# Kernel tuning notes

Hardware: AMD Instinct MI355X
Metric: run time of the kernel (lower is better)

## Reference

```python
import jax, jax.numpy as jnp
import numpy as np

N, E, D_IN, D, D_OUT = 100000, 3200000, 16, 128, 16
LN_EPS = 1e-5


def setup_inputs() -> dict:
    key = jax.random.key(0)
    ks = jax.random.split(key, 10)
    s = lambda fan_in: 1.0 / np.sqrt(fan_in)
    return {
        "X": jax.random.normal(ks[0], (N, D_IN), jnp.float32),
        "W_enc0": jax.random.uniform(ks[1], (D_IN, D), jnp.float32, -s(D_IN), s(D_IN)),
        "b_enc0": jnp.zeros((D,), jnp.float32),
        "W_enc1": jax.random.uniform(ks[2], (D, D), jnp.float32, -s(D), s(D)),
        "b_enc1": jnp.zeros((D,), jnp.float32),
        "W_conv": jax.random.uniform(ks[3], (D, D), jnp.float32, -s(D), s(D)),
        "b_conv": jnp.zeros((D,), jnp.float32),
        "ln_g": jnp.ones((D,), jnp.float32),
        "ln_b": jnp.zeros((D,), jnp.float32),
        "W_dec0": jax.random.uniform(ks[4], (D, D), jnp.float32, -s(D), s(D)),
        "b_dec0": jnp.zeros((D,), jnp.float32),
        "W_dec1": jax.random.uniform(ks[5], (D, D_OUT), jnp.float32, -s(D), s(D)),
        "b_dec1": jnp.zeros((D_OUT,), jnp.float32),
        "edge_index": jax.random.randint(ks[6], (2, E), 0, N, jnp.int64),
        "msg_steps": 3,
    }


def _layer_norm(x, g, b):
    mu = jnp.mean(x, axis=-1, keepdims=True)
    var = jnp.mean((x - mu) ** 2, axis=-1, keepdims=True)
    return (x - mu) * jax.lax.rsqrt(var + LN_EPS) * g + b


def reference(X, W_enc0, b_enc0, W_enc1, b_enc1, W_conv, b_conv, ln_g, ln_b,
              W_dec0, b_dec0, W_dec1, b_dec1, edge_index, msg_steps):
    n = X.shape[0]
    # --- PyG GCNConv normalization: add self-loops, symmetric deg norm ---
    loops = jnp.arange(n, dtype=edge_index.dtype)
    row = jnp.concatenate([edge_index[0], loops])  # source nodes [E+N]
    col = jnp.concatenate([edge_index[1], loops])  # target nodes [E+N]
    deg = jax.ops.segment_sum(jnp.ones_like(col, jnp.float32), col, num_segments=n)
    dinv = jnp.where(deg > 0, jax.lax.rsqrt(deg), 0.0)
    norm = dinv[row] * dinv[col]  # [E+N]

    # --- encoder MLP (relu between layers, none after last) ---
    x = jax.nn.relu(X @ W_enc0 + b_enc0)
    x = x @ W_enc1 + b_enc1

    # --- message-passing loop: x = LN(x + GCNConv(x)) ---
    for _ in range(msg_steps):
        h = x @ W_conv                          # [N, D] linear first (GCNConv)
        msg = h[row] * norm[:, None]            # gather + scale  [E+N, D]
        agg = jax.ops.segment_sum(msg, col, num_segments=n) + b_conv
        x = _layer_norm(x + agg, ln_g, ln_b)

    # --- decoder MLP ---
    x = jax.nn.relu(x @ W_dec0 + b_dec0)
    x = x @ W_dec1 + b_dec1
    return x
```

## Files before the change

kernel.cpp:

```cpp
#include <hip/hip_runtime.h>

#define N_NODES 100000
#define NEDGE   3200000
#define DIN     16
#define DIM     128
#define DOUT    16
#define LN_EPS  1e-5f
#define NBINS   391
#define CHUNK   4096
#define NPB     782
#define XS_STRIDE 136
#define GGRID   1024
#define FP8_SCALE  64.0f
#define FP8_ISCALE 0.015625f

typedef __attribute__((ext_vector_type(8))) __bf16 bfrag_t;
typedef __attribute__((ext_vector_type(4))) float facc_t;
typedef __attribute__((ext_vector_type(2))) float fx2;

static __device__ __forceinline__ facc_t mfma16(bfrag_t a, bfrag_t b, facc_t c) {
    return __builtin_amdgcn_mfma_f32_16x16x32_bf16(a, b, c, 0, 0, 0);
}

static __device__ __forceinline__ unsigned f2bf(float f) {
    unsigned u = __float_as_uint(f);
    return (u + 0x7fffu + ((u >> 16) & 1u)) >> 16;
}
static __device__ __forceinline__ float bf_lo(unsigned u) { return __uint_as_float(u << 16); }
static __device__ __forceinline__ float bf_hi(unsigned u) { return __uint_as_float(u & 0xFFFF0000u); }

static __device__ __forceinline__ unsigned char f2fp8(float v) {
    return (unsigned char)__builtin_amdgcn_cvt_pk_fp8_f32(v, v, 0u, false);
}


__global__ __launch_bounds__(256) void k_hist2(const int* __restrict__ col,
                                               int* __restrict__ chunkhist) {
    __shared__ int lh[NBINS];
    int tid = threadIdx.x;
    for (int b = tid; b < NBINS; b += 256) lh[b] = 0;
    __syncthreads();
    int e0 = blockIdx.x * CHUNK;
    int e1 = e0 + CHUNK; if (e1 > NEDGE) e1 = NEDGE;
    for (int e = e0 + tid; e < e1; e += 256)
        atomicAdd(&lh[col[e] >> 8], 1);
    __syncthreads();
    int* out = chunkhist + (size_t)blockIdx.x * NBINS;
    for (int b = tid; b < NBINS; b += 256) out[b] = lh[b];
}

__global__ __launch_bounds__(256) void k_scanA(const int* __restrict__ chunkhist,
                                               int* __restrict__ bintot) {
    __shared__ int sh[256];
    int b = blockIdx.x, t = threadIdx.x;
    int s = 0;
    for (int c = t; c < NPB; c += 256) s += chunkhist[(size_t)c * NBINS + b];
    sh[t] = s;
    __syncthreads();
    for (int off = 128; off > 0; off >>= 1) {
        if (t < off) sh[t] += sh[t + off];
        __syncthreads();
    }
    if (t == 0) bintot[b] = sh[0];
}

__global__ __launch_bounds__(512) void k_scanB(const int* __restrict__ bintot,
                                               int* __restrict__ binbase) {
    __shared__ int sh[512];
    int t = threadIdx.x;
    int v = (t < NBINS) ? bintot[t] : 0;
    sh[t] = v;
    __syncthreads();
    for (int off = 1; off < 512; off <<= 1) {
        int a = (t >= off) ? sh[t - off] : 0;
        __syncthreads();
        sh[t] += a;
        __syncthreads();
    }
    if (t < NBINS) binbase[t] = sh[t] - v;
    if (t == 0) binbase[NBINS] = NEDGE;
}

__global__ __launch_bounds__(256) void k_scanC(const int* __restrict__ chunkhist,
                                               const int* __restrict__ binbase,
                                               int* __restrict__ chunkbase) {
    __shared__ int sh[256];
    __shared__ int carry_s;
    int b = blockIdx.x, t = threadIdx.x;
    if (t == 0) carry_s = binbase[b];
    __syncthreads();
    const int ROUNDS = (NPB + 255) / 256;
    for (int r = 0; r < ROUNDS; r++) {
        int idx = r * 256 + t;
        int v = (idx < NPB) ? chunkhist[(size_t)idx * NBINS + b] : 0;
        sh[t] = v;
        __syncthreads();
        for (int off = 1; off < 256; off <<= 1) {
            int a = (t >= off) ? sh[t - off] : 0;
            __syncthreads();
            sh[t] += a;
            __syncthreads();
        }
        int incl = sh[t];
        int carry = carry_s;
        if (idx < NPB) chunkbase[(size_t)idx * NBINS + b] = carry + incl - v;
        __syncthreads();
        if (t == 255) carry_s = carry + incl;
        __syncthreads();
    }
}

__global__ __launch_bounds__(256) void k_binpass2(const int* __restrict__ row, const int* __restrict__ col,
                                                  const int* __restrict__ chunkbase,
                                                  unsigned* __restrict__ pairs) {
    __shared__ int lbase[NBINS], lofs[NBINS];
    int tid = threadIdx.x;
    const int* cb = chunkbase + (size_t)blockIdx.x * NBINS;
    for (int b = tid; b < NBINS; b += 256) { lbase[b] = cb[b]; lofs[b] = 0; }
    __syncthreads();
    int e0 = blockIdx.x * CHUNK;
    int e1 = e0 + CHUNK; if (e1 > NEDGE) e1 = NEDGE;
    for (int e = e0 + tid; e < e1; e += 256) {
        int c = col[e];
        int b = c >> 8;
        int pos = atomicAdd(&lofs[b], 1);
        pairs[lbase[b] + pos] = ((unsigned)(c & 255) << 17) | (unsigned)row[e];
    }
}

__global__ __launch_bounds__(256) void k_csr2(const unsigned* __restrict__ pairs,
                                              const int* __restrict__ binbase,
                                              int* __restrict__ indptr, float* __restrict__ dinv,
                                              int* __restrict__ rows_s) {
    __shared__ int lcnt[256], lptr[256], lofs[256];
    __shared__ int wsum[4];
    int tid = threadIdx.x;
    int b = blockIdx.x;
    int n0 = b << 8;
    int base = binbase[b], end = binbase[b + 1];
    lcnt[tid] = 0; lofs[tid] = 0;
    __syncthreads();
    for (int s = base + tid; s < end; s += 256)
        atomicAdd(&lcnt[pairs[s] >> 17], 1);
    __syncthreads();
    int v = lcnt[tid];
    int lane = tid & 63, w = tid >> 6;
    int s = v;
    for (int off = 1; off < 64; off <<= 1) {
        int t = __shfl_up(s, off);
        if (lane >= off) s += t;
    }
    if (lane == 63) wsum[w] = s;
    __syncthreads();
    int add = 0;
    for (int k = 0; k < w; k++) add += wsum[k];
    int excl = add + s - v;
    lptr[tid] = excl;
    int node = n0 + tid;
    if (node < N_NODES) {
        indptr[node] = base + excl;
        dinv[node] = rsqrtf((float)(v + 1));
    }
    if (b == NBINS - 1 && tid == 0) indptr[N_NODES] = NEDGE;
    __syncthreads();
    for (int s2 = base + tid; s2 < end; s2 += 256) {
        unsigned p = pairs[s2];
        int cl = p >> 17;
        int r  = p & 0x1FFFF;
        int dst = base + lptr[cl] + atomicAdd(&lofs[cl], 1);
        rows_s[dst] = r;
    }
}

template<int NC, int NT>
static __device__ __forceinline__ void load_bfrags(const float* __restrict__ W, int colbase,
                                                   int lane, bfrag_t B[NT][4]) {
    int q = lane >> 4, nn = lane & 15;
    #pragma unroll
    for (int nt = 0; nt < NT; nt++) {
        int col = colbase + 16 * nt + nn;
        #pragma unroll
        for (int kc = 0; kc < 4; kc++) {
            int k0 = 32 * kc + 8 * q;
            bfrag_t f;
            #pragma unroll
            for (int j = 0; j < 8; j++)
                f[j] = (__bf16)W[(size_t)(k0 + j) * NC + col];
            B[nt][kc] = f;
        }
    }
}

static __device__ __forceinline__ void stage_bf(const unsigned short* __restrict__ src_base,
                                                short* __restrict__ xs, int tid) {
    int r = tid >> 3, s = tid & 7;
    const uint4* src = (const uint4*)(src_base + (size_t)r * DIM + 16 * s);
    uint4 a = src[0], b = src[1];
    *(uint4*)&xs[r * XS_STRIDE + 16 * s] = a;
    *(uint4*)&xs[r * XS_STRIDE + 16 * s + 8] = b;
}

static __device__ __forceinline__ void conv_tail(const short* __restrict__ ys, bfrag_t B[2][4],
                                                 const float* __restrict__ dinv, int nb,
                                                 int lane, int wv, unsigned char* __restrict__ hs_out) {
    int q = lane >> 4, nn = lane & 15;
    facc_t a2[2][2] = {};
    #pragma unroll
    for (int kc = 0; kc < 4; kc++) {
        bfrag_t a0 = *(const bfrag_t*)&ys[nn * XS_STRIDE + 32 * kc + 8 * q];
        bfrag_t a1 = *(const bfrag_t*)&ys[(16 + nn) * XS_STRIDE + 32 * kc + 8 * q];
        a2[0][0] = mfma16(a0, B[0][kc], a2[0][0]);
        a2[0][1] = mfma16(a0, B[1][kc], a2[0][1]);
        a2[1][0] = mfma16(a1, B[0][kc], a2[1][0]);
        a2[1][1] = mfma16(a1, B[1][kc], a2[1][1]);
    }
    #pragma unroll
    for (int mt = 0; mt < 2; mt++)
        #pragma unroll
        for (int r = 0; r < 4; r++) {
            int node = nb + 16 * mt + 4 * q + r;
            float d64 = dinv[node] * FP8_SCALE;
            #pragma unroll
            for (int nt = 0; nt < 2; nt++)
                hs_out[(size_t)node * DIM + 32 * wv + 16 * nt + nn] =
                    f2fp8(a2[mt][nt][r] * d64);
        }
}


__global__ __launch_bounds__(256) void k_encC(const float* __restrict__ X,
                                              const float* __restrict__ W0, const float* __restrict__ b0,
                                              const float* __restrict__ W1, const float* __restrict__ b1,
                                              const float* __restrict__ Wc, const float* __restrict__ dinv,
                                              unsigned short* __restrict__ xo, unsigned char* __restrict__ hs_out) {
    __shared__ short xs[32 * XS_STRIDE];
    __shared__ float W0s[DIN * DIM];
    __shared__ float b0s[DIM];
    int tid = threadIdx.x, lane = tid & 63, wv = tid >> 6;
    for (int i = tid; i < DIN * DIM / 4; i += 256) ((float4*)W0s)[i] = ((const float4*)W0)[i];
    if (tid < DIM) b0s[tid] = b0[tid];
    bfrag_t B[2][4];
    load_bfrags<DIM, 2>(W1, 32 * wv, lane, B);
    bfrag_t Bc[2][4];
    load_bfrags<DIM, 2>(Wc, 32 * wv, lane, Bc);
    int q = lane >> 4, nn = lane & 15;
    float bias[2] = { b1[32 * wv + nn], b1[32 * wv + 16 + nn] };
    const int ngroups = N_NODES / 32;
    for (int g = blockIdx.x; g < ngroups; g += gridDim.x) {
        int n0 = g * 32;
        __syncthreads();
        {
            int r = tid >> 3, s = tid & 7;
            float xr[DIN];
            const float4* xsrc = (const float4*)(X + (size_t)(n0 + r) * DIN);
            #pragma unroll
            for (int i = 0; i < 4; i++) {
                float4 v = xsrc[i];
                xr[4*i] = v.x; xr[4*i+1] = v.y; xr[4*i+2] = v.z; xr[4*i+3] = v.w;
            }
            unsigned pk[8];
            #pragma unroll
            for (int cc = 0; cc < 16; cc += 2) {
                int c0 = 16 * s + cc;
                float a0 = b0s[c0], a1 = b0s[c0 + 1];
                #pragma unroll
                for (int k = 0; k < DIN; k++) {
                    float2 w = *(const float2*)&W0s[k * DIM + c0];
                    a0 += xr[k] * w.x; a1 += xr[k] * w.y;
                }
                pk[cc >> 1] = f2bf(fmaxf(a0, 0.f)) | (f2bf(fmaxf(a1, 0.f)) << 16);
            }
            *(uint4*)&xs[r * XS_STRIDE + 16 * s] = *(uint4*)&pk[0];
            *(uint4*)&xs[r * XS_STRIDE + 16 * s + 8] = *(uint4*)&pk[4];
        }
        __syncthreads();
        facc_t acc[2][2];
        #pragma unroll
        for (int mt = 0; mt < 2; mt++)
            #pragma unroll
            for (int nt = 0; nt < 2; nt++)
                acc[mt][nt] = (facc_t){bias[nt], bias[nt], bias[nt], bias[nt]};
        #pragma unroll
        for (int kc = 0; kc < 4; kc++) {
            bfrag_t a0 = *(const bfrag_t*)&xs[nn * XS_STRIDE + 32 * kc + 8 * q];
            bfrag_t a1 = *(const bfrag_t*)&xs[(16 + nn) * XS_STRIDE + 32 * kc + 8 * q];
            acc[0][0] = mfma16(a0, B[0][kc], acc[0][0]);
            acc[0][1] = mfma16(a0, B[1][kc], acc[0][1]);
            acc[1][0] = mfma16(a1, B[0][kc], acc[1][0]);
            acc[1][1] = mfma16(a1, B[1][kc], acc[1][1]);
        }
        __syncthreads();
        #pragma unroll
        for (int mt = 0; mt < 2; mt++)
            #pragma unroll
            for (int r = 0; r < 4; r++) {
                int node = n0 + 16 * mt + 4 * q + r;
                int nl = 16 * mt + 4 * q + r;
                #pragma unroll
                for (int nt = 0; nt < 2; nt++) {
                    int col = 32 * wv + 16 * nt + nn;
                    unsigned short bv = (unsigned short)f2bf(acc[mt][nt][r]);
                    xo[(size_t)node * DIM + col] = bv;
                    xs[nl * XS_STRIDE + col] = (short)bv;
                }
            }
        __syncthreads();
        conv_tail(xs, Bc, dinv, n0, lane, wv, hs_out);
    }
}


__global__ __launch_bounds__(256) void k_convM(const unsigned short* __restrict__ xi,
                                               const float* __restrict__ W,
                                               const float* __restrict__ dinv,
                                               unsigned char* __restrict__ hs) {
    __shared__ short xs[32 * XS_STRIDE];
    int tid = threadIdx.x, lane = tid & 63, wv = tid >> 6;
    bfrag_t B[2][4];
    load_bfrags<DIM, 2>(W, 32 * wv, lane, B);
    const int ngroups = N_NODES / 32;
    for (int g = blockIdx.x; g < ngroups; g += gridDim.x) {
        int n0 = g * 32;
        __syncthreads();
        stage_bf(xi + (size_t)n0 * DIM, xs, tid);
        __syncthreads();
        conv_tail(xs, B, dinv, n0, lane, wv, hs);
    }
}


static __device__ __forceinline__ void accp(fx2* __restrict__ acc, uint2 u) {
    acc[0] += __builtin_amdgcn_cvt_pk_f32_fp8(u.x, false);
    acc[1] += __builtin_amdgcn_cvt_pk_f32_fp8(u.x, true);
    acc[2] += __builtin_amdgcn_cvt_pk_f32_fp8(u.y, false);
    acc[3] += __builtin_amdgcn_cvt_pk_f32_fp8(u.y, true);
}

__global__ __launch_bounds__(256) void k_agg_ln(const uint2* __restrict__ hs2, uint4* __restrict__ x4,
                                                const float* __restrict__ dinv,
                                                const int* __restrict__ indptr,
                                                const int* __restrict__ rows_s,
                                                const float* __restrict__ bconv,
                                                const float* __restrict__ g_, const float* __restrict__ b_) {
    int v = (blockIdx.x * blockDim.x + threadIdx.x) >> 6;
    int lane = threadIdx.x & 63;
    if (v >= N_NODES) return;
    int sub = lane >> 4, part = lane & 15;
    const char* hsb = (const char*)hs2;
    unsigned pb = (unsigned)part << 3;
    fx2 acc[4];
    #pragma unroll
    for (int j = 0; j < 4; j++) acc[j] = (fx2){0.f, 0.f};
    {
        uint2 u = *(const uint2*)(hsb + (((unsigned)v << 7) | pb));
        if (sub == 0) accp(acc, u);
    }
    int beg = indptr[v], end = indptr[v + 1];
    for (int base = beg; base < end; base += 64) {
        int m = end - base; if (m > 64) m = 64;
        int r0 = rows_s[base + (lane < m ? lane : m - 1)];
        int k = 0;
        for (; k + 16 <= m; k += 16) {
            int ia = __shfl(r0, k + sub);
            int ib = __shfl(r0, k + 4 + sub);
            int ic = __shfl(r0, k + 8 + sub);
            int id = __shfl(r0, k + 12 + sub);
            uint2 ua = *(const uint2*)(hsb + (((unsigned)ia << 7) | pb));
            uint2 ub = *(const uint2*)(hsb + (((unsigned)ib << 7) | pb));
            uint2 uc = *(const uint2*)(hsb + (((unsigned)ic << 7) | pb));
            uint2 ud = *(const uint2*)(hsb + (((unsigned)id << 7) | pb));
            accp(acc, ua); accp(acc, ub); accp(acc, uc); accp(acc, ud);
        }
        for (; k + 4 <= m; k += 4) {
            int i = __shfl(r0, k + sub);
            uint2 u = *(const uint2*)(hsb + (((unsigned)i << 7) | pb));
            accp(acc, u);
        }
        if (k < m) {
            int kk = k + sub;
            bool valid = kk < m;
            int i = __shfl(r0, valid ? kk : m - 1);
            uint2 u = *(const uint2*)(hsb + (((unsigned)i << 7) | pb));
            if (valid) accp(acc, u);
        }
    }
    float a8[8];
    #pragma unroll
    for (int j = 0; j < 4; j++) { a8[2 * j] = acc[j][0]; a8[2 * j + 1] = acc[j][1]; }
    #pragma unroll
    for (int j = 0; j < 8; j++) {
        a8[j] += __shfl_xor(a8[j], 16);
        a8[j] += __shfl_xor(a8[j], 32);
    }
    float dvs = dinv[v] * FP8_ISCALE;
    float y[8];
    {
        uint4 xu = x4[(size_t)v * 16 + part];
        const float4* bc = (const float4*)(bconv + 8 * part);
        float4 b0 = bc[0], b1 = bc[1];
        y[0] = bf_lo(xu.x) + dvs * a8[0] + b0.x; y[1] = bf_hi(xu.x) + dvs * a8[1] + b0.y;
        y[2] = bf_lo(xu.y) + dvs * a8[2] + b0.z; y[3] = bf_hi(xu.y) + dvs * a8[3] + b0.w;
        y[4] = bf_lo(xu.z) + dvs * a8[4] + b1.x; y[5] = bf_hi(xu.z) + dvs * a8[5] + b1.y;
        y[6] = bf_lo(xu.w) + dvs * a8[6] + b1.z; y[7] = bf_hi(xu.w) + dvs * a8[7] + b1.w;
    }
    float s = 0.f, s2 = 0.f;
    #pragma unroll
    for (int j = 0; j < 8; j++) { s += y[j]; s2 += y[j] * y[j]; }
    #pragma unroll
    for (int off = 1; off < 16; off <<= 1) {
        s += __shfl_xor(s, off);
        s2 += __shfl_xor(s2, off);
    }
    float mu = s * (1.f / 128.f);
    float rstd = rsqrtf(s2 * (1.f / 128.f) - mu * mu + LN_EPS);
    if (sub == 0) {
        const float4* gp = (const float4*)(g_ + 8 * part);
        const float4* bp = (const float4*)(b_ + 8 * part);
        float4 g0 = gp[0], g1 = gp[1];
        float4 bb0 = bp[0], bb1 = bp[1];
        float o[8];
        o[0] = (y[0] - mu) * rstd * g0.x + bb0.x;
        o[1] = (y[1] - mu) * rstd * g0.y + bb0.y;
        o[2] = (y[2] - mu) * rstd * g0.z + bb0.z;
        o[3] = (y[3] - mu) * rstd * g0.w + bb0.w;
        o[4] = (y[4] - mu) * rstd * g1.x + bb1.x;
        o[5] = (y[5] - mu) * rstd * g1.y + bb1.y;
        o[6] = (y[6] - mu) * rstd * g1.z + bb1.z;
        o[7] = (y[7] - mu) * rstd * g1.w + bb1.w;
        uint4 ow;
        ow.x = f2bf(o[0]) | (f2bf(o[1]) << 16);
        ow.y = f2bf(o[2]) | (f2bf(o[3]) << 16);
        ow.z = f2bf(o[4]) | (f2bf(o[5]) << 16);
        ow.w = f2bf(o[6]) | (f2bf(o[7]) << 16);
        x4[(size_t)v * 16 + part] = ow;
    }
}


__global__ __launch_bounds__(256) void k_decM(const unsigned short* __restrict__ xi,
                                              const float* __restrict__ W0, const float* __restrict__ b0f,
                                              const float* __restrict__ W1, const float* __restrict__ b1f,
                                              float* __restrict__ out) {
    __shared__ short xs[32 * XS_STRIDE];
    int tid = threadIdx.x, lane = tid & 63, wv = tid >> 6;
    bfrag_t B0[2][4];
    load_bfrags<DIM, 2>(W0, 32 * wv, lane, B0);
    int q = lane >> 4, nn = lane & 15;
    bfrag_t B1[4];
    #pragma unroll
    for (int kc = 0; kc < 4; kc++) {
        int k0 = 32 * kc + 8 * q;
        bfrag_t f;
        #pragma unroll
        for (int j = 0; j < 8; j++)
            f[j] = (__bf16)W1[(size_t)(k0 + j) * DOUT + nn];
        B1[kc] = f;
    }
    float bias0[2] = { b0f[32 * wv + nn], b0f[32 * wv + 16 + nn] };
    float bias1 = b1f[nn];
    const int ngroups = N_NODES / 32;
    for (int g = blockIdx.x; g < ngroups; g += gridDim.x) {
        int n0 = g * 32;
        __syncthreads();
        stage_bf(xi + (size_t)n0 * DIM, xs, tid);
        __syncthreads();
        facc_t acc[2][2];
        #pragma unroll
        for (int mt = 0; mt < 2; mt++)
            #pragma unroll
            for (int nt = 0; nt < 2; nt++)
                acc[mt][nt] = (facc_t){bias0[nt], bias0[nt], bias0[nt], bias0[nt]};
        #pragma unroll
        for (int kc = 0; kc < 4; kc++) {
            bfrag_t a0 = *(const bfrag_t*)&xs[nn * XS_STRIDE + 32 * kc + 8 * q];
            bfrag_t a1 = *(const bfrag_t*)&xs[(16 + nn) * XS_STRIDE + 32 * kc + 8 * q];
            acc[0][0] = mfma16(a0, B0[0][kc], acc[0][0]);
            acc[0][1] = mfma16(a0, B0[1][kc], acc[0][1]);
            acc[1][0] = mfma16(a1, B0[0][kc], acc[1][0]);
            acc[1][1] = mfma16(a1, B0[1][kc], acc[1][1]);
        }
        __syncthreads();
        #pragma unroll
        for (int mt = 0; mt < 2; mt++)
            #pragma unroll
            for (int nt = 0; nt < 2; nt++)
                #pragma unroll
                for (int r = 0; r < 4; r++) {
                    int nl = 16 * mt + 4 * q + r;
                    int col = 32 * wv + 16 * nt + nn;
                    xs[nl * XS_STRIDE + col] = (short)f2bf(fmaxf(acc[mt][nt][r], 0.f));
                }
        __syncthreads();
        if (wv < 2) {
            facc_t acc2 = (facc_t){bias1, bias1, bias1, bias1};
            #pragma unroll
            for (int kc = 0; kc < 4; kc++) {
                bfrag_t a = *(const bfrag_t*)&xs[(16 * wv + nn) * XS_STRIDE + 32 * kc + 8 * q];
                acc2 = mfma16(a, B1[kc], acc2);
            }
            #pragma unroll
            for (int r = 0; r < 4; r++) {
                int node = n0 + 16 * wv + 4 * q + r;
                out[(size_t)node * DOUT + nn] = acc2[r];
            }
        }
    }
}


extern "C" void kernel_launch(void* const* d_in, const int* in_sizes, int n_in,
                              void* d_out, int out_size, void* d_ws, size_t ws_size,
                              hipStream_t stream) {
    const float* X      = (const float*)d_in[0];
    const float* W_enc0 = (const float*)d_in[1];
    const float* b_enc0 = (const float*)d_in[2];
    const float* W_enc1 = (const float*)d_in[3];
    const float* b_enc1 = (const float*)d_in[4];
    const float* W_conv = (const float*)d_in[5];
    const float* b_conv = (const float*)d_in[6];
    const float* ln_g   = (const float*)d_in[7];
    const float* ln_b   = (const float*)d_in[8];
    const float* W_dec0 = (const float*)d_in[9];
    const float* b_dec0 = (const float*)d_in[10];
    const float* W_dec1 = (const float*)d_in[11];
    const float* b_dec1 = (const float*)d_in[12];
    const int*   erow   = (const int*)d_in[13];
    const int*   ecol   = erow + NEDGE;
    float* out = (float*)d_out;

    unsigned short* x         = (unsigned short*)d_ws;
    unsigned char*  hs        = (unsigned char*)(x + (size_t)N_NODES * DIM);
    float*          dinv      = (float*)(hs + (size_t)N_NODES * DIM);
    int*            indptr    = (int*)(dinv + N_NODES);
    int*            binbase   = indptr + N_NODES + 8;
    int*            bintot    = binbase + NBINS + 9;
    int*            chunkhist = bintot + NBINS + 8;
    int*            chunkbase = chunkhist + NPB * NBINS + 8;
    int*            rows_s    = chunkbase + NPB * NBINS + 8;
    unsigned*       pairs     = (unsigned*)hs;

    k_hist2   <<<NPB, 256, 0, stream>>>(ecol, chunkhist);
    k_scanA   <<<NBINS, 256, 0, stream>>>(chunkhist, bintot);
    k_scanB   <<<1, 512, 0, stream>>>(bintot, binbase);
    k_scanC   <<<NBINS, 256, 0, stream>>>(chunkhist, binbase, chunkbase);
    k_binpass2<<<NPB, 256, 0, stream>>>(erow, ecol, chunkbase, pairs);
    k_csr2    <<<NBINS, 256, 0, stream>>>(pairs, binbase, indptr, dinv, rows_s);

    k_encC<<<GGRID, 256, 0, stream>>>(X, W_enc0, b_enc0, W_enc1, b_enc1, W_conv, dinv, x, hs);

    k_agg_ln<<<N_NODES / 4, 256, 0, stream>>>((const uint2*)hs, (uint4*)x, dinv, indptr, rows_s,
                                              b_conv, ln_g, ln_b);
    k_convM <<<GGRID, 256, 0, stream>>>(x, W_conv, dinv, hs);
    k_agg_ln<<<N_NODES / 4, 256, 0, stream>>>((const uint2*)hs, (uint4*)x, dinv, indptr, rows_s,
                                              b_conv, ln_g, ln_b);
    k_convM <<<GGRID, 256, 0, stream>>>(x, W_conv, dinv, hs);
    k_agg_ln<<<N_NODES / 4, 256, 0, stream>>>((const uint2*)hs, (uint4*)x, dinv, indptr, rows_s,
                                              b_conv, ln_g, ln_b);

    k_decM<<<GGRID, 256, 0, stream>>>(x, W_dec0, b_dec0, W_dec1, b_dec1, out);
}
```

Baseline: 467.2 us.

## Fuse conv linear into aggregation+LayerNorm kernel with double-buffered hs

Folds the per-step conv matmul (x @ W_conv, scaled by dinv, quantized to fp8) into the aggregate/LayerNorm kernel. Each 4-node block stages its normalized rows in LDS and runs MFMA to produce next-step hs. Two hs buffers alternate because other blocks still read the old hs while new values are written. This removes two convM launches and the re-read of x, but each block now reloads W_conv fragments from global memory for only 4 nodes, and the 16x16 MFMA tiles are mostly wasted on 4 rows.

```diff
diff --git a/kernel.cpp b/kernel.cpp
--- a/kernel.cpp
+++ b/kernel.cpp
@@ -189,15 +189,6 @@
             B[nt][kc] = f;
         }
     }
-}
-
-static __device__ __forceinline__ void stage_bf(const unsigned short* __restrict__ src_base,
-                                                short* __restrict__ xs, int tid) {
-    int r = tid >> 3, s = tid & 7;
-    const uint4* src = (const uint4*)(src_base + (size_t)r * DIM + 16 * s);
-    uint4 a = src[0], b = src[1];
-    *(uint4*)&xs[r * XS_STRIDE + 16 * s] = a;
-    *(uint4*)&xs[r * XS_STRIDE + 16 * s + 8] = b;
 }
 
 static __device__ __forceinline__ void conv_tail(const short* __restrict__ ys, bfrag_t B[2][4],
@@ -310,25 +301,6 @@
 }
 
 
-__global__ __launch_bounds__(256) void k_convM(const unsigned short* __restrict__ xi,
-                                               const float* __restrict__ W,
-                                               const float* __restrict__ dinv,
-                                               unsigned char* __restrict__ hs) {
-    __shared__ short xs[32 * XS_STRIDE];
-    int tid = threadIdx.x, lane = tid & 63, wv = tid >> 6;
-    bfrag_t B[2][4];
-    load_bfrags<DIM, 2>(W, 32 * wv, lane, B);
-    const int ngroups = N_NODES / 32;
-    for (int g = blockIdx.x; g < ngroups; g += gridDim.x) {
-        int n0 = g * 32;
-        __syncthreads();
-        stage_bf(xi + (size_t)n0 * DIM, xs, tid);
-        __syncthreads();
-        conv_tail(xs, B, dinv, n0, lane, wv, hs);
-    }
-}
-
-
 static __device__ __forceinline__ void accp(fx2* __restrict__ acc, uint2 u) {
     acc[0] += __builtin_amdgcn_cvt_pk_f32_fp8(u.x, false);
     acc[1] += __builtin_amdgcn_cvt_pk_f32_fp8(u.x, true);
@@ -336,15 +308,17 @@
     acc[3] += __builtin_amdgcn_cvt_pk_f32_fp8(u.y, true);
 }
 
-__global__ __launch_bounds__(256) void k_agg_ln(const uint2* __restrict__ hs2, uint4* __restrict__ x4,
-                                                const float* __restrict__ dinv,
-                                                const int* __restrict__ indptr,
-                                                const int* __restrict__ rows_s,
-                                                const float* __restrict__ bconv,
-                                                const float* __restrict__ g_, const float* __restrict__ b_) {
-    int v = (blockIdx.x * blockDim.x + threadIdx.x) >> 6;
+template<int FUSE_CONV>
+static __device__ __forceinline__ void agg_body(const uint2* hs2, uint4* x4,
+                                                const float* dinv, const int* indptr,
+                                                const int* rows_s, const float* bconv,
+                                                const float* g_, const float* b_,
+                                                const float* Wc, unsigned char* hs_out,
+                                                short* os) {
+    int wv = threadIdx.x >> 6;
+    int n0 = blockIdx.x * 4;
+    int v = n0 + wv;
     int lane = threadIdx.x & 63;
-    if (v >= N_NODES) return;
     int sub = lane >> 4, part = lane & 15;
     const char* hsb = (const char*)hs2;
     unsigned pb = (unsigned)part << 3;
@@ -433,9 +407,64 @@
         ow.z = f2bf(o[4]) | (f2bf(o[5]) << 16);
         ow.w = f2bf(o[6]) | (f2bf(o[7]) << 16);
         x4[(size_t)v * 16 + part] = ow;
-    }
-}
-
+        if (FUSE_CONV)
+            *(uint4*)&os[wv * XS_STRIDE + 8 * part] = ow;
+    }
+    if (FUSE_CONV) {
+        __syncthreads();
+        bfrag_t Bc[2][4];
+        load_bfrags<DIM, 2>(Wc, 32 * wv, lane, Bc);
+        facc_t a2[2];
+        a2[0] = (facc_t){0.f, 0.f, 0.f, 0.f};
+        a2[1] = (facc_t){0.f, 0.f, 0.f, 0.f};
+        #pragma unroll
+        for (int kc = 0; kc < 4; kc++) {
+            bfrag_t a = *(const bfrag_t*)&os[(lane & 3) * XS_STRIDE + 32 * kc + 8 * sub];
+            a2[0] = mfma16(a, Bc[0][kc], a2[0]);
+            a2[1] = mfma16(a, Bc[1][kc], a2[1]);
+        }
+        if (sub == 0) {
+            #pragma unroll
+            for (int r = 0; r < 4; r++) {
+                int node = n0 + r;
+                float d64 = dinv[node] * FP8_SCALE;
+                hs_out[(size_t)node * DIM + 32 * wv + part]      = f2fp8(a2[0][r] * d64);
+                hs_out[(size_t)node * DIM + 32 * wv + 16 + part] = f2fp8(a2[1][r] * d64);
+            }
+        }
+    }
+}
+
+__global__ __launch_bounds__(256) void k_agg_cv(const uint2* __restrict__ hs2, uint4* __restrict__ x4,
+                                                const float* __restrict__ dinv,
+                                                const int* __restrict__ indptr,
+                                                const int* __restrict__ rows_s,
+                                                const float* __restrict__ bconv,
+                                                const float* __restrict__ g_, const float* __restrict__ b_,
+                                                const float* __restrict__ Wc,
+                                                unsigned char* __restrict__ hs_out) {
+    __shared__ short os[4 * XS_STRIDE];
+    agg_body<1>(hs2, x4, dinv, indptr, rows_s, bconv, g_, b_, Wc, hs_out, os);
+}
+
+__global__ __launch_bounds__(256) void k_agg_ln(const uint2* __restrict__ hs2, uint4* __restrict__ x4,
+                                                const float* __restrict__ dinv,
+                                                const int* __restrict__ indptr,
+                                                const int* __restrict__ rows_s,
+                                                const float* __restrict__ bconv,
+                                                const float* __restrict__ g_, const float* __restrict__ b_) {
+    agg_body<0>(hs2, x4, dinv, indptr, rows_s, bconv, g_, b_, nullptr, nullptr, nullptr);
+}
+
+
+static __device__ __forceinline__ void stage_bf(const unsigned short* __restrict__ src_base,
+                                                short* __restrict__ xs, int tid) {
+    int r = tid >> 3, s = tid & 7;
+    const uint4* src = (const uint4*)(src_base + (size_t)r * DIM + 16 * s);
+    uint4 a = src[0], b = src[1];
+    *(uint4*)&xs[r * XS_STRIDE + 16 * s] = a;
+    *(uint4*)&xs[r * XS_STRIDE + 16 * s + 8] = b;
+}
 
 __global__ __launch_bounds__(256) void k_decM(const unsigned short* __restrict__ xi,
                                               const float* __restrict__ W0, const float* __restrict__ b0f,
@@ -529,15 +558,16 @@
     float* out = (float*)d_out;
 
     unsigned short* x         = (unsigned short*)d_ws;
-    unsigned char*  hs        = (unsigned char*)(x + (size_t)N_NODES * DIM);
-    float*          dinv      = (float*)(hs + (size_t)N_NODES * DIM);
+    unsigned char*  hs_a      = (unsigned char*)(x + (size_t)N_NODES * DIM);
+    unsigned char*  hs_b      = hs_a + (size_t)N_NODES * DIM;
+    float*          dinv      = (float*)(hs_b + (size_t)N_NODES * DIM);
     int*            indptr    = (int*)(dinv + N_NODES);
     int*            binbase   = indptr + N_NODES + 8;
     int*            bintot    = binbase + NBINS + 9;
     int*            chunkhist = bintot + NBINS + 8;
     int*            chunkbase = chunkhist + NPB * NBINS + 8;
     int*            rows_s    = chunkbase + NPB * NBINS + 8;
-    unsigned*       pairs     = (unsigned*)hs;
+    unsigned*       pairs     = (unsigned*)hs_b;
 
     k_hist2   <<<NPB, 256, 0, stream>>>(ecol, chunkhist);
     k_scanA   <<<NBINS, 256, 0, stream>>>(chunkhist, bintot);
@@ -546,16 +576,14 @@
     k_binpass2<<<NPB, 256, 0, stream>>>(erow, ecol, chunkbase, pairs);
     k_csr2    <<<NBINS, 256, 0, stream>>>(pairs, binbase, indptr, dinv, rows_s);
 
-    k_encC<<<GGRID, 256, 0, stream>>>(X, W_enc0, b_enc0, W_enc1, b_enc1, W_conv, dinv, x, hs);
-
-    k_agg_ln<<<N_NODES / 4, 256, 0, stream>>>((const uint2*)hs, (uint4*)x, dinv, indptr, rows_s,
+    k_encC<<<GGRID, 256, 0, stream>>>(X, W_enc0, b_enc0, W_enc1, b_enc1, W_conv, dinv, x, hs_a);
+
+    k_agg_cv<<<N_NODES / 4, 256, 0, stream>>>((const uint2*)hs_a, (uint4*)x, dinv, indptr, rows_s,
+                                              b_conv, ln_g, ln_b, W_conv, hs_b);
+    k_agg_cv<<<N_NODES / 4, 256, 0, stream>>>((const uint2*)hs_b, (uint4*)x, dinv, indptr, rows_s,
+                                              b_conv, ln_g, ln_b, W_conv, hs_a);
+    k_agg_ln<<<N_NODES / 4, 256, 0, stream>>>((const uint2*)hs_a, (uint4*)x, dinv, indptr, rows_s,
                                               b_conv, ln_g, ln_b);
-    k_convM <<<GGRID, 256, 0, stream>>>(x, W_conv, dinv, hs);
-    k_agg_ln<<<N_NODES / 4, 256, 0, stream>>>((const uint2*)hs, (uint4*)x, dinv, indptr, rows_s,
-                                              b_conv, ln_g, ln_b);
-    k_convM <<<GGRID, 256, 0, stream>>>(x, W_conv, dinv, hs);
-    k_agg_ln<<<N_NODES / 4, 256, 0, stream>>>((const uint2*)hs, (uint4*)x, dinv, indptr, rows_s,
-                                              b_conv, ln_g, ln_b);
 
     k_decM<<<GGRID, 256, 0, stream>>>(x, W_dec0, b_dec0, W_dec1, b_dec1, out);
 }
```

After: 589.9 us. +26.3%, slower.
